# Optimization experiments

Hardware: AMD Instinct MI355X
Metric: run time of the kernel (lower is better)

## Reference

```python
import jax, jax.numpy as jnp
import numpy as np

N = 100_000   # nodes
E = 3_200_000 # edges (avg degree 32)
D = 256       # gnn width
H = 128       # mlp hidden
C = 5         # num classes


def _gcn_conv(x, W, b, src, dst, norm, n):
    # PyG GCNConv: h = x @ W^T, then symmetric-normalized scatter-add over edges
    h = x @ W.T
    msgs = norm[:, None] * h[src]                      # [E+N, out]
    out = jax.ops.segment_sum(msgs, dst, num_segments=n)
    return out + b


def setup_inputs() -> dict:
    key = jax.random.key(0)
    ks = jax.random.split(key, 8)
    x = jax.random.normal(ks[0], (N, D), dtype=jnp.float32)
    edge_index = jax.random.randint(ks[1], (2, E), 0, N, dtype=jnp.int32)
    def lin(k, out_d, in_d):
        return jax.random.normal(k, (out_d, in_d), dtype=jnp.float32) / np.sqrt(in_d).astype(np.float32)
    return {
        "x": x,
        "edge_index": edge_index,
        "W1": lin(ks[2], D, D), "b1": jnp.zeros((D,), jnp.float32),
        "W2": lin(ks[3], D, D), "b2": jnp.zeros((D,), jnp.float32),
        "Wm1": lin(ks[4], H, D), "bm1": jnp.zeros((H,), jnp.float32),
        "Wm2": lin(ks[5], C, H), "bm2": jnp.zeros((C,), jnp.float32),
    }


def reference(x, edge_index, W1, b1, W2, b2, Wm1, bm1, Wm2, bm2):
    # add self-loops (PyG GCNConv default add_self_loops=True)
    loop = jnp.arange(N, dtype=edge_index.dtype)
    src = jnp.concatenate([edge_index[0], loop])
    dst = jnp.concatenate([edge_index[1], loop])
    # symmetric normalization: deg from destination index (flow source_to_target)
    deg = jax.ops.segment_sum(jnp.ones(src.shape[0], x.dtype), dst, num_segments=N)
    dinv = jnp.where(deg > 0, jax.lax.rsqrt(deg), 0.0)
    norm = dinv[src] * dinv[dst]                       # [E+N]

    h = _gcn_conv(x, W1, b1, src, dst, norm, N)
    h = _gcn_conv(h, W2, b2, src, dst, norm, N)
    # MLP head (no activations in original module)
    h = h @ Wm1.T + bm1
    h = h @ Wm2.T + bm2
    return h
```

## Files before the change

### kernel.cpp

```cpp
#include <hip/hip_runtime.h>

#define N_NODES 100000
#define N_EDGES 3200000
#define DIM 256
#define HID 128
#define NCLS 5
#define NBUCK 782
#define P1B 256
#define EPB 12500
#define HPKC 16

__global__ void k_zero(int* p, int n) {
    int i = blockIdx.x * 256 + threadIdx.x;
    if (i < n) p[i] = 0;
}

template<int K>
__global__ __launch_bounds__(256) void k_hp_stage(const float* __restrict__ A,
        const float* __restrict__ B, float* __restrict__ OUT)
{
    int t = threadIdx.x;
    int k0 = blockIdx.x * HPKC;
    float acc[NCLS] = {0, 0, 0, 0, 0};
    #pragma unroll
    for (int kk = 0; kk < HPKC; ++kk) {
        int k = k0 + kk;
        float b = B[k * DIM + t];
        #pragma unroll
        for (int c = 0; c < NCLS; ++c) acc[c] += A[c * K + k] * b;
    }
    #pragma unroll
    for (int c = 0; c < NCLS; ++c) atomicAdd(&OUT[c * DIM + t], acc[c]);
}

__global__ __launch_bounds__(320) void k_hp_bias(const float* __restrict__ Wc,
        const float* __restrict__ W2c, const float* __restrict__ Wm2,
        const float* __restrict__ b1, const float* __restrict__ b2,
        const float* __restrict__ bm1, const float* __restrict__ bm2,
        float* __restrict__ bq, float* __restrict__ bc2)
{
    int c = threadIdx.x >> 6;
    int lane = threadIdx.x & 63;
    float s = 0.0f;
    for (int i = lane; i < DIM; i += 64) s += W2c[c * DIM + i] * b1[i];
    #pragma unroll
    for (int off = 32; off > 0; off >>= 1) s += __shfl_xor(s, off);
    float b = 0.0f;
    for (int k = lane; k < HID; k += 64) b += Wm2[c * HID + k] * bm1[k];
    for (int o = lane; o < DIM; o += 64) b += Wc[c * DIM + o] * b2[o];
    #pragma unroll
    for (int off = 32; off > 0; off >>= 1) b += __shfl_xor(b, off);
    if (lane == 0) { bq[c] = s; bc2[c] = bm2[c] + b; }
}

__global__ __launch_bounds__(256) void k_p1hist(const int* __restrict__ dst,
        int* __restrict__ gcount, int* __restrict__ blockbase)
{
    __shared__ int lh[NBUCK];
    int tid = threadIdx.x;
    for (int i = tid; i < NBUCK; i += 256) lh[i] = 0;
    __syncthreads();
    int s = blockIdx.x * EPB, e1 = s + EPB;
    for (int e = s + tid; e < e1; e += 256) atomicAdd(&lh[dst[e] >> 7], 1);
    __syncthreads();
    for (int i = tid; i < NBUCK; i += 256) {
        int c = lh[i];
        blockbase[blockIdx.x * NBUCK + i] = c ? atomicAdd(&gcount[i], c) : 0;
    }
}
__global__ __launch_bounds__(256) void k_scanb(const int* __restrict__ gcount,
        int* __restrict__ gbase)
{
    __shared__ int sdata[256];
    __shared__ int s_base;
    int tid = threadIdx.x;
    if (tid == 0) s_base = 0;
    __syncthreads();
    for (int base = 0; base < NBUCK; base += 256) {
        int i = base + tid;
        int v = (i < NBUCK) ? gcount[i] : 0;
        sdata[tid] = v;
        __syncthreads();
        #pragma unroll
        for (int off = 1; off < 256; off <<= 1) {
            int t = (tid >= off) ? sdata[tid - off] : 0;
            __syncthreads();
            sdata[tid] += t;
            __syncthreads();
        }
        if (i < NBUCK) gbase[i] = s_base + sdata[tid] - v;
        int total = sdata[255];
        __syncthreads();
        if (tid == 0) s_base += total;
        __syncthreads();
    }
    if (tid == 0) gbase[NBUCK] = N_EDGES;
}
__global__ __launch_bounds__(256) void k_p1scatter(const int* __restrict__ src,
        const int* __restrict__ dst, const int* __restrict__ gbase,
        const int* __restrict__ blockbase, unsigned* __restrict__ ebuf)
{
    __shared__ int lh[NBUCK];
    int tid = threadIdx.x;
    for (int i = tid; i < NBUCK; i += 256) lh[i] = 0;
    __syncthreads();
    int s = blockIdx.x * EPB, e1 = s + EPB;
    for (int e = s + tid; e < e1; e += 256) {
        int d = dst[e];
        int b = d >> 7;
        int r = atomicAdd(&lh[b], 1);
        int pos = gbase[b] + blockbase[blockIdx.x * NBUCK + b] + r;
        ebuf[pos] = ((unsigned)src[e] << 7) | (unsigned)(d & 127);
    }
}
__global__ __launch_bounds__(256) void k_p2(const unsigned* __restrict__ ebuf,
        const int* __restrict__ gbase, int* __restrict__ rowptr,
        float* __restrict__ dinv, int* __restrict__ esrc)
{
    __shared__ int c[128];
    __shared__ int sdata[128];
    __shared__ int cur[128];
    int tid = threadIdx.x, b = blockIdx.x;
    if (tid < 128) c[tid] = 0;
    __syncthreads();
    int s = gbase[b], e1 = gbase[b + 1];
    for (int e = s + tid; e < e1; e += 256) atomicAdd(&c[ebuf[e] & 127u], 1);
    __syncthreads();
    int cnt = (tid < 128) ? c[tid] : 0;
    if (tid < 128) sdata[tid] = cnt;
    __syncthreads();
    #pragma unroll
    for (int off = 1; off < 128; off <<= 1) {
        int t = (tid >= off && tid < 128) ? sdata[tid - off] : 0;
        __syncthreads();
        if (tid < 128) sdata[tid] += t;
        __syncthreads();
    }
    if (tid < 128) {
        int rp = gbase[b] + sdata[tid] - cnt;
        cur[tid] = rp;
        int node = b * 128 + tid;
        if (node < N_NODES) {
            rowptr[node] = rp;
            dinv[node] = rsqrtf((float)(cnt + 1));
        }
    }
    if (b == 0 && tid == 0) rowptr[N_NODES] = N_EDGES;
    __syncthreads();
    for (int e = s + tid; e < e1; e += 256) {
        unsigned p = ebuf[e];
        int pos = atomicAdd(&cur[p & 127u], 1);
        esrc[pos] = (int)(p >> 7);
    }
}

__global__ __launch_bounds__(256) void k_q(const float* __restrict__ x,
        const float* __restrict__ Wq, const float* __restrict__ dinv,
        float* __restrict__ qbuf)
{
    int wid = (blockIdx.x * 256 + threadIdx.x) >> 6;
    int lane = threadIdx.x & 63;
    int lane4 = lane * 4;
    int nwaves = gridDim.x * 4;
    float4 w[NCLS];
    #pragma unroll
    for (int c = 0; c < NCLS; ++c) w[c] = *(const float4*)(Wq + c * DIM + lane4);
    for (int d = wid; d < N_NODES; d += nwaves) {
        float4 xv = *(const float4*)(x + (size_t)d * DIM + lane4);
        float p[NCLS];
        #pragma unroll
        for (int c = 0; c < NCLS; ++c) {
            float s = xv.x * w[c].x + xv.y * w[c].y + xv.z * w[c].z + xv.w * w[c].w;
            #pragma unroll
            for (int off = 32; off > 0; off >>= 1) s += __shfl_xor(s, off);
            p[c] = s;
        }
        if (lane == 0) {
            float dv = dinv[d];
            #pragma unroll
            for (int c = 0; c < NCLS; ++c) qbuf[(size_t)d * 8 + c] = dv * p[c];
        }
    }
}

template<int MODE>
__global__ __launch_bounds__(256) void k_gather5(const float* __restrict__ in,
        const int* __restrict__ rowptr, const int* __restrict__ esrc,
        const float* __restrict__ dinv, const float* __restrict__ bias,
        float* __restrict__ out, int ostride)
{
    int gid = blockIdx.x * 256 + threadIdx.x;
    int d = gid >> 2, sub = gid & 3;
    if (d >= N_NODES) return;
    float acc0 = 0, acc1 = 0, acc2 = 0, acc3 = 0, acc4 = 0;
    int r0 = rowptr[d], r1 = rowptr[d + 1];
    for (int j = r0 + sub; j < r1; j += 4) {
        int s = esrc[j];
        float4 v = *(const float4*)(in + (size_t)s * 8);
        float v4 = in[(size_t)s * 8 + 4];
        acc0 += v.x; acc1 += v.y; acc2 += v.z; acc3 += v.w; acc4 += v4;
    }
    if (sub == 0) {
        float4 v = *(const float4*)(in + (size_t)d * 8);
        float v4 = in[(size_t)d * 8 + 4];
        acc0 += v.x; acc1 += v.y; acc2 += v.z; acc3 += v.w; acc4 += v4;
    }
    #pragma unroll
    for (int off = 1; off < 4; off <<= 1) {
        acc0 += __shfl_xor(acc0, off);
        acc1 += __shfl_xor(acc1, off);
        acc2 += __shfl_xor(acc2, off);
        acc3 += __shfl_xor(acc3, off);
        acc4 += __shfl_xor(acc4, off);
    }
    if (sub == 0) {
        float dv = dinv[d];
        float scale = (MODE == 1) ? dv * dv : dv;
        float bs = (MODE == 1) ? dv : 1.0f;
        out[(size_t)d * ostride + 0] = scale * acc0 + bs * bias[0];
        out[(size_t)d * ostride + 1] = scale * acc1 + bs * bias[1];
        out[(size_t)d * ostride + 2] = scale * acc2 + bs * bias[2];
        out[(size_t)d * ostride + 3] = scale * acc3 + bs * bias[3];
        out[(size_t)d * ostride + 4] = scale * acc4 + bs * bias[4];
    }
}

extern "C" void kernel_launch(void* const* d_in, const int* in_sizes, int n_in,
                              void* d_out, int out_size, void* d_ws, size_t ws_size,
                              hipStream_t stream)
{
    const float* x   = (const float*)d_in[0];
    const int*   ei  = (const int*)d_in[1];
    const float* W1  = (const float*)d_in[2];
    const float* b1  = (const float*)d_in[3];
    const float* W2  = (const float*)d_in[4];
    const float* b2  = (const float*)d_in[5];
    const float* Wm1 = (const float*)d_in[6];
    const float* bm1 = (const float*)d_in[7];
    const float* Wm2 = (const float*)d_in[8];
    const float* bm2 = (const float*)d_in[9];
    float* out = (float*)d_out;
    const int* src = ei;
    const int* dst = ei + N_EDGES;

    char* ws = (char*)d_ws;
    float* dinv   = (float*)(ws + 0x0000000);
    int* rowptr   = (int*)  (ws + 0x0080000);
    int* esrc     = (int*)  (ws + 0x0200000);
    float* hpw    = (float*)(ws + 0x0F00000);
    float* Wq     = hpw;
    float* Wc     = hpw + NCLS * DIM;
    float* W2c    = hpw + 2 * NCLS * DIM;
    float* bq     = (float*)(ws + 0x0F10000);
    float* bc2    = (float*)(ws + 0x0F11000);
    float* qbuf   = (float*)(ws + 0x1000000);
    float* tbuf   = (float*)(ws + 0x1400000);
    unsigned* ebuf = (unsigned*)(ws + 0x2000000);
    int* blockbase = (int*) (ws + 0x2E00000);
    int* gcount    = (int*) (ws + 0x2F00000);
    int* gbase     = (int*) (ws + 0x2F02000);

    k_zero<<<(3 * NCLS * DIM + 255) / 256, 256, 0, stream>>>((int*)hpw, 3 * NCLS * DIM);
    k_hp_stage<HID><<<HID / HPKC, 256, 0, stream>>>(Wm2, Wm1, Wc);
    k_hp_stage<DIM><<<DIM / HPKC, 256, 0, stream>>>(Wc, W2, W2c);
    k_hp_bias<<<1, 320, 0, stream>>>(Wc, W2c, Wm2, b1, b2, bm1, bm2, bq, bc2);
    k_hp_stage<DIM><<<DIM / HPKC, 256, 0, stream>>>(W2c, W1, Wq);

    k_zero<<<(NBUCK + 255) / 256, 256, 0, stream>>>(gcount, NBUCK);
    k_p1hist<<<P1B, 256, 0, stream>>>(dst, gcount, blockbase);
    k_scanb<<<1, 256, 0, stream>>>(gcount, gbase);
    k_p1scatter<<<P1B, 256, 0, stream>>>(src, dst, gbase, blockbase, ebuf);
    k_p2<<<NBUCK, 256, 0, stream>>>(ebuf, gbase, rowptr, dinv, esrc);

    k_q<<<2048, 256, 0, stream>>>(x, Wq, dinv, qbuf);

    const int GB = (N_NODES * 4 + 255) / 256;
    k_gather5<1><<<GB, 256, 0, stream>>>(qbuf, rowptr, esrc, dinv, bq, tbuf, 8);
    k_gather5<0><<<GB, 256, 0, stream>>>(tbuf, rowptr, esrc, dinv, bc2, out, NCLS);
}
```

Before: 370.6 us.

## Replace CSR build with bucketed edges and LDS-atomic aggregation

Drops the second sorting pass that built a full CSR (rowptr/esrc). Edges are instead bucketed by destination into 256-node buckets. Degrees are counted per bucket, and both propagation steps accumulate the 5-wide messages into shared-memory float atomics per bucket. This removes the per-node scatter pass and the esrc buffer, at the cost of LDS atomic contention and float-atomic ordering nondeterminism. Bucket size and block sizes for the histogram and scatter kernels are also enlarged.

```diff
diff --git a/kernel.cpp b/kernel.cpp
--- a/kernel.cpp
+++ b/kernel.cpp
@@ -5,7 +5,9 @@
 #define DIM 256
 #define HID 128
 #define NCLS 5
-#define NBUCK 782
+#define BSH 8
+#define BSZ 256
+#define NBUCK 391
 #define P1B 256
 #define EPB 12500
 #define HPKC 16
@@ -53,17 +55,17 @@
     if (lane == 0) { bq[c] = s; bc2[c] = bm2[c] + b; }
 }
 
-__global__ __launch_bounds__(256) void k_p1hist(const int* __restrict__ dst,
+__global__ __launch_bounds__(1024) void k_p1hist(const int* __restrict__ dst,
         int* __restrict__ gcount, int* __restrict__ blockbase)
 {
     __shared__ int lh[NBUCK];
     int tid = threadIdx.x;
-    for (int i = tid; i < NBUCK; i += 256) lh[i] = 0;
+    for (int i = tid; i < NBUCK; i += 1024) lh[i] = 0;
     __syncthreads();
     int s = blockIdx.x * EPB, e1 = s + EPB;
-    for (int e = s + tid; e < e1; e += 256) atomicAdd(&lh[dst[e] >> 7], 1);
-    __syncthreads();
-    for (int i = tid; i < NBUCK; i += 256) {
+    for (int e = s + tid; e < e1; e += 1024) atomicAdd(&lh[dst[e] >> BSH], 1);
+    __syncthreads();
+    for (int i = tid; i < NBUCK; i += 1024) {
         int c = lh[i];
         blockbase[blockIdx.x * NBUCK + i] = c ? atomicAdd(&gcount[i], c) : 0;
     }
@@ -96,61 +98,37 @@
     }
     if (tid == 0) gbase[NBUCK] = N_EDGES;
 }
-__global__ __launch_bounds__(256) void k_p1scatter(const int* __restrict__ src,
+__global__ __launch_bounds__(1024) void k_p1scatter(const int* __restrict__ src,
         const int* __restrict__ dst, const int* __restrict__ gbase,
         const int* __restrict__ blockbase, unsigned* __restrict__ ebuf)
 {
     __shared__ int lh[NBUCK];
     int tid = threadIdx.x;
-    for (int i = tid; i < NBUCK; i += 256) lh[i] = 0;
+    for (int i = tid; i < NBUCK; i += 1024) lh[i] = 0;
     __syncthreads();
     int s = blockIdx.x * EPB, e1 = s + EPB;
-    for (int e = s + tid; e < e1; e += 256) {
+    for (int e = s + tid; e < e1; e += 1024) {
         int d = dst[e];
-        int b = d >> 7;
+        int b = d >> BSH;
         int r = atomicAdd(&lh[b], 1);
         int pos = gbase[b] + blockbase[blockIdx.x * NBUCK + b] + r;
-        ebuf[pos] = ((unsigned)src[e] << 7) | (unsigned)(d & 127);
-    }
-}
-__global__ __launch_bounds__(256) void k_p2(const unsigned* __restrict__ ebuf,
-        const int* __restrict__ gbase, int* __restrict__ rowptr,
-        float* __restrict__ dinv, int* __restrict__ esrc)
-{
-    __shared__ int c[128];
-    __shared__ int sdata[128];
-    __shared__ int cur[128];
+        ebuf[pos] = ((unsigned)src[e] << 8) | (unsigned)(d & 255);
+    }
+}
+
+__global__ __launch_bounds__(512) void k_deg(const unsigned* __restrict__ ebuf,
+        const int* __restrict__ gbase, float* __restrict__ dinv)
+{
+    __shared__ int c[BSZ];
     int tid = threadIdx.x, b = blockIdx.x;
-    if (tid < 128) c[tid] = 0;
+    if (tid < BSZ) c[tid] = 0;
     __syncthreads();
     int s = gbase[b], e1 = gbase[b + 1];
-    for (int e = s + tid; e < e1; e += 256) atomicAdd(&c[ebuf[e] & 127u], 1);
-    __syncthreads();
-    int cnt = (tid < 128) ? c[tid] : 0;
-    if (tid < 128) sdata[tid] = cnt;
-    __syncthreads();
-    #pragma unroll
-    for (int off = 1; off < 128; off <<= 1) {
-        int t = (tid >= off && tid < 128) ? sdata[tid - off] : 0;
-        __syncthreads();
-        if (tid < 128) sdata[tid] += t;
-        __syncthreads();
-    }
-    if (tid < 128) {
-        int rp = gbase[b] + sdata[tid] - cnt;
-        cur[tid] = rp;
-        int node = b * 128 + tid;
-        if (node < N_NODES) {
-            rowptr[node] = rp;
-            dinv[node] = rsqrtf((float)(cnt + 1));
-        }
-    }
-    if (b == 0 && tid == 0) rowptr[N_NODES] = N_EDGES;
-    __syncthreads();
-    for (int e = s + tid; e < e1; e += 256) {
-        unsigned p = ebuf[e];
-        int pos = atomicAdd(&cur[p & 127u], 1);
-        esrc[pos] = (int)(p >> 7);
+    for (int e = s + tid; e < e1; e += 512) atomicAdd(&c[ebuf[e] & 255u], 1);
+    __syncthreads();
+    if (tid < BSZ) {
+        int node = b * BSZ + tid;
+        if (node < N_NODES) dinv[node] = rsqrtf((float)(c[tid] + 1));
     }
 }
 
@@ -184,44 +162,53 @@
 }
 
 template<int MODE>
-__global__ __launch_bounds__(256) void k_gather5(const float* __restrict__ in,
-        const int* __restrict__ rowptr, const int* __restrict__ esrc,
+__global__ __launch_bounds__(512) void k_gab(const float* __restrict__ in,
+        const unsigned* __restrict__ ebuf, const int* __restrict__ gbase,
         const float* __restrict__ dinv, const float* __restrict__ bias,
-        float* __restrict__ out, int ostride)
-{
-    int gid = blockIdx.x * 256 + threadIdx.x;
-    int d = gid >> 2, sub = gid & 3;
-    if (d >= N_NODES) return;
-    float acc0 = 0, acc1 = 0, acc2 = 0, acc3 = 0, acc4 = 0;
-    int r0 = rowptr[d], r1 = rowptr[d + 1];
-    for (int j = r0 + sub; j < r1; j += 4) {
-        int s = esrc[j];
-        float4 v = *(const float4*)(in + (size_t)s * 8);
-        float v4 = in[(size_t)s * 8 + 4];
-        acc0 += v.x; acc1 += v.y; acc2 += v.z; acc3 += v.w; acc4 += v4;
-    }
-    if (sub == 0) {
-        float4 v = *(const float4*)(in + (size_t)d * 8);
-        float v4 = in[(size_t)d * 8 + 4];
-        acc0 += v.x; acc1 += v.y; acc2 += v.z; acc3 += v.w; acc4 += v4;
-    }
-    #pragma unroll
-    for (int off = 1; off < 4; off <<= 1) {
-        acc0 += __shfl_xor(acc0, off);
-        acc1 += __shfl_xor(acc1, off);
-        acc2 += __shfl_xor(acc2, off);
-        acc3 += __shfl_xor(acc3, off);
-        acc4 += __shfl_xor(acc4, off);
-    }
-    if (sub == 0) {
-        float dv = dinv[d];
-        float scale = (MODE == 1) ? dv * dv : dv;
-        float bs = (MODE == 1) ? dv : 1.0f;
-        out[(size_t)d * ostride + 0] = scale * acc0 + bs * bias[0];
-        out[(size_t)d * ostride + 1] = scale * acc1 + bs * bias[1];
-        out[(size_t)d * ostride + 2] = scale * acc2 + bs * bias[2];
-        out[(size_t)d * ostride + 3] = scale * acc3 + bs * bias[3];
-        out[(size_t)d * ostride + 4] = scale * acc4 + bs * bias[4];
+        float* __restrict__ out)
+{
+    __shared__ float acc[BSZ][NCLS];
+    int tid = threadIdx.x, b = blockIdx.x;
+    for (int i = tid; i < BSZ * NCLS; i += 512) (&acc[0][0])[i] = 0.0f;
+    __syncthreads();
+    int s = gbase[b], e1 = gbase[b + 1];
+    for (int e = s + tid; e < e1; e += 512) {
+        unsigned p = ebuf[e];
+        const float* q = in + (size_t)(p >> 8) * 8;
+        int n = p & 255u;
+        float4 v = *(const float4*)q;
+        float v4 = q[4];
+        atomicAdd(&acc[n][0], v.x);
+        atomicAdd(&acc[n][1], v.y);
+        atomicAdd(&acc[n][2], v.z);
+        atomicAdd(&acc[n][3], v.w);
+        atomicAdd(&acc[n][4], v4);
+    }
+    __syncthreads();
+    if (tid < BSZ) {
+        int node = b * BSZ + tid;
+        if (node < N_NODES) {
+            float dv = dinv[node];
+            float sc = MODE ? dv * dv : dv;
+            float bs = MODE ? dv : 1.0f;
+            const float* q = in + (size_t)node * 8;
+            #pragma unroll
+            for (int c = 0; c < NCLS; ++c)
+                acc[tid][c] = sc * (acc[tid][c] + q[c]) + bs * bias[c];
+        }
+    }
+    __syncthreads();
+    if (MODE) {
+        for (int i = tid; i < BSZ * 8; i += 512) {
+            int n = i >> 3, c = i & 7;
+            int node = b * BSZ + n;
+            if (node < N_NODES) out[(size_t)node * 8 + c] = (c < NCLS) ? acc[n][c] : 0.0f;
+        }
+    } else {
+        for (int i = tid; i < BSZ * NCLS; i += 512) {
+            size_t idx = (size_t)b * BSZ * NCLS + i;
+            if (idx < (size_t)N_NODES * NCLS) out[idx] = (&acc[0][0])[i];
+        }
     }
 }
 
@@ -245,20 +232,18 @@
 
     char* ws = (char*)d_ws;
     float* dinv   = (float*)(ws + 0x0000000);
-    int* rowptr   = (int*)  (ws + 0x0080000);
-    int* esrc     = (int*)  (ws + 0x0200000);
-    float* hpw    = (float*)(ws + 0x0F00000);
+    float* hpw    = (float*)(ws + 0x0080000);
     float* Wq     = hpw;
     float* Wc     = hpw + NCLS * DIM;
     float* W2c    = hpw + 2 * NCLS * DIM;
-    float* bq     = (float*)(ws + 0x0F10000);
-    float* bc2    = (float*)(ws + 0x0F11000);
-    float* qbuf   = (float*)(ws + 0x1000000);
-    float* tbuf   = (float*)(ws + 0x1400000);
-    unsigned* ebuf = (unsigned*)(ws + 0x2000000);
-    int* blockbase = (int*) (ws + 0x2E00000);
-    int* gcount    = (int*) (ws + 0x2F00000);
-    int* gbase     = (int*) (ws + 0x2F02000);
+    float* bq     = (float*)(ws + 0x0090000);
+    float* bc2    = (float*)(ws + 0x0091000);
+    float* qbuf   = (float*)(ws + 0x0100000);
+    float* tbuf   = (float*)(ws + 0x0500000);
+    unsigned* ebuf = (unsigned*)(ws + 0x0900000);
+    int* blockbase = (int*) (ws + 0x1600000);
+    int* gcount    = (int*) (ws + 0x1700000);
+    int* gbase     = (int*) (ws + 0x1702000);
 
     k_zero<<<(3 * NCLS * DIM + 255) / 256, 256, 0, stream>>>((int*)hpw, 3 * NCLS * DIM);
     k_hp_stage<HID><<<HID / HPKC, 256, 0, stream>>>(Wm2, Wm1, Wc);
@@ -267,14 +252,13 @@
     k_hp_stage<DIM><<<DIM / HPKC, 256, 0, stream>>>(W2c, W1, Wq);
 
     k_zero<<<(NBUCK + 255) / 256, 256, 0, stream>>>(gcount, NBUCK);
-    k_p1hist<<<P1B, 256, 0, stream>>>(dst, gcount, blockbase);
+    k_p1hist<<<P1B, 1024, 0, stream>>>(dst, gcount, blockbase);
     k_scanb<<<1, 256, 0, stream>>>(gcount, gbase);
-    k_p1scatter<<<P1B, 256, 0, stream>>>(src, dst, gbase, blockbase, ebuf);
-    k_p2<<<NBUCK, 256, 0, stream>>>(ebuf, gbase, rowptr, dinv, esrc);
+    k_p1scatter<<<P1B, 1024, 0, stream>>>(src, dst, gbase, blockbase, ebuf);
+    k_deg<<<NBUCK, 512, 0, stream>>>(ebuf, gbase, dinv);
 
     k_q<<<2048, 256, 0, stream>>>(x, Wq, dinv, qbuf);
 
-    const int GB = (N_NODES * 4 + 255) / 256;
-    k_gather5<1><<<GB, 256, 0, stream>>>(qbuf, rowptr, esrc, dinv, bq, tbuf, 8);
-    k_gather5<0><<<GB, 256, 0, stream>>>(tbuf, rowptr, esrc, dinv, bc2, out, NCLS);
-}
+    k_gab<1><<<NBUCK, 512, 0, stream>>>(qbuf, ebuf, gbase, dinv, bq, tbuf);
+    k_gab<0><<<NBUCK, 512, 0, stream>>>(tbuf, ebuf, gbase, dinv, bc2, out);
+}
```

After: 475.7 us. 1.28x slower.
